# Kernel tuning notes

Hardware: AMD Instinct MI355X
Metric: run time of the kernel (lower is better)

## Reference

```python
import jax, jax.numpy as jnp
import numpy as np

N_NODES = 20000
IN_C = 512
OUT_C = 128
HEADS = 4
N_EDGES = 320000
NEG_SLOPE = 0.2


def setup_inputs() -> dict:
    key = jax.random.key(0)
    ks = jax.random.split(key, 10)
    x = jax.random.normal(ks[0], (N_NODES, IN_C), dtype=jnp.float32)
    edge_index = jax.random.randint(ks[1], (2, N_EDGES), 0, N_NODES, dtype=jnp.int64)
    s = 0.05
    return {
        "x": x,
        "edge_index": edge_index,
        "W1": jax.random.normal(ks[2], (IN_C, HEADS * OUT_C), dtype=jnp.float32) * s,
        "a_src1": jax.random.normal(ks[3], (HEADS, OUT_C), dtype=jnp.float32) * s,
        "a_dst1": jax.random.normal(ks[4], (HEADS, OUT_C), dtype=jnp.float32) * s,
        "b1": jnp.zeros((HEADS * OUT_C,), dtype=jnp.float32),
        "W2": jax.random.normal(ks[5], (HEADS * OUT_C, 1 * OUT_C), dtype=jnp.float32) * s,
        "a_src2": jax.random.normal(ks[6], (1, OUT_C), dtype=jnp.float32) * s,
        "a_dst2": jax.random.normal(ks[7], (1, OUT_C), dtype=jnp.float32) * s,
        "b2": jnp.zeros((OUT_C,), dtype=jnp.float32),
    }


def gat_conv(x, src, dst, W, a_src, a_dst, b, heads, out_c, concat):
    N = x.shape[0]
    h = (x @ W).reshape(N, heads, out_c)            # [N,H,C]
    al_src = jnp.sum(h * a_src, axis=-1)            # [N,H]
    al_dst = jnp.sum(h * a_dst, axis=-1)            # [N,H]
    e = jax.nn.leaky_relu(al_src[src] + al_dst[dst], NEG_SLOPE)  # [E,H]
    # segment softmax over edges grouped by destination node
    e_max = jax.ops.segment_max(e, dst, num_segments=N)         # [N,H]
    e = jnp.exp(e - e_max[dst])
    denom = jax.ops.segment_sum(e, dst, num_segments=N)         # [N,H]
    alpha = e / (denom[dst] + 1e-16)                             # [E,H]
    msg = h[src] * alpha[:, :, None]                             # [E,H,C]
    out = jax.ops.segment_sum(msg, dst, num_segments=N)          # [N,H,C]
    out = out.reshape(N, heads * out_c) if concat else jnp.mean(out, axis=1)
    return out + b


def reference(x, edge_index, W1, a_src1, a_dst1, b1, W2, a_src2, a_dst2, b2):
    N = x.shape[0]
    # PyG GATConv adds self-loops by default
    loops = jnp.arange(N, dtype=edge_index.dtype)
    src = jnp.concatenate([edge_index[0], loops])
    dst = jnp.concatenate([edge_index[1], loops])
    h = gat_conv(x, src, dst, W1, a_src1, a_dst1, b1, HEADS, OUT_C, concat=True)
    h = jax.nn.elu(h)
    return gat_conv(h, src, dst, W2, a_src2, a_dst2, b2, 1, OUT_C, concat=False)
```

## Files before the change

kernel.cpp:

```cpp
#include <hip/hip_runtime.h>
#include <hip/hip_bf16.h>

typedef __hip_bfloat16 bf16;
typedef __bf16 bf16x8 __attribute__((ext_vector_type(8)));
typedef float f32x4 __attribute__((ext_vector_type(4)));

#define NEG_SLOPE 0.2f
#define F32_THRESH 256


__device__ __forceinline__ bool is_f32(const int* fcnt) { return *fcnt > F32_THRESH; }

__device__ __forceinline__ float ld_f(const void* p, long long i, bool f32) {
    return f32 ? ((const float*)p)[i] : __bfloat162float(((const bf16*)p)[i]);
}

__device__ __forceinline__ float b2f(unsigned hs) {
    return __uint_as_float(hs << 16);
}

__device__ __forceinline__ unsigned pack_bf2(float a, float b) {
    union { bf16 h[2]; unsigned u; } p;
    p.h[0] = __float2bfloat16(a);
    p.h[1] = __float2bfloat16(b);
    return p.u;
}

__device__ __forceinline__ void load_lds16(const void* g, void* l) {
    __builtin_amdgcn_global_load_lds(
        (const __attribute__((address_space(1))) void*)g,
        (__attribute__((address_space(3))) void*)l, 16, 0, 0);
}

template <int CPL> struct FV;
template <> struct FV<8> {
    uint4 v;
    __device__ __forceinline__ void load(const bf16* p) { v = *(const uint4*)p; }
    __device__ __forceinline__ void fma(float* acc, float w) const {
        unsigned uu[4] = {v.x, v.y, v.z, v.w};
#pragma unroll
        for (int q = 0; q < 4; q++) {
            acc[2 * q] += w * b2f(uu[q] & 0xFFFFu);
            acc[2 * q + 1] += w * b2f(uu[q] >> 16);
        }
    }
};
template <> struct FV<2> {
    unsigned v;
    __device__ __forceinline__ void load(const bf16* p) { v = *(const unsigned*)p; }
    __device__ __forceinline__ void fma(float* acc, float w) const {
        acc[0] += w * b2f(v & 0xFFFFu);
        acc[1] += w * b2f(v >> 16);
    }
};


__global__ void k_probe(const unsigned* xw, long long nw, const int* idx, int n_half,
                        int* cnt, int* iflag) {
    long long t = blockIdx.x * (long long)blockDim.x + threadIdx.x;
    long long stride = (long long)gridDim.x * blockDim.x;
    int c = 0;
    for (long long i = t; i < nw; i += stride)
        if ((xw[i] & 0x7F80u) == 0x7F80u) c++;
    if (c) atomicAdd(cnt, c);
    int any = 0;
    for (long long i = t; i < n_half; i += stride)
        if (idx[2 * i + 1] != 0) any = 1;
    if (any) atomicOr(iflag, 1);
}


__device__ __forceinline__ int edge_val(const void* idx, long long i, int is64) {
    return is64 ? (int)((const long long*)idx)[i] : ((const int*)idx)[i];
}

__global__ void k_count(const void* idx, const int* iflag, int E0, int N, int* deg) {
    int e = blockIdx.x * blockDim.x + threadIdx.x;
    if (e >= E0 + N) return;
    int is64 = (*iflag == 0);
    int d = (e < E0) ? edge_val(idx, (long long)E0 + e, is64) : (e - E0);
    if ((unsigned)d >= (unsigned)N) d = 0;
    atomicAdd(&deg[d], 1);
}

__global__ __launch_bounds__(1024) void k_scan(const int* deg, int* rowptr, int N) {
    __shared__ int part[1024];
    int t = threadIdx.x;
    int chunk = (N + 1023) / 1024;
    int s = t * chunk, e = min(N, s + chunk);
    int sum = 0;
    for (int i = s; i < e; i++) sum += deg[i];
    part[t] = sum;
    __syncthreads();
    for (int off = 1; off < 1024; off <<= 1) {
        int v = (t >= off) ? part[t - off] : 0;
        __syncthreads();
        part[t] += v;
        __syncthreads();
    }
    int run = (t == 0) ? 0 : part[t - 1];
    for (int i = s; i < e; i++) { rowptr[i] = run; run += deg[i]; }
    if (t == 1023) rowptr[N] = part[1023];
}

__global__ void k_scatter(const void* idx, const int* iflag, int E0, int N,
                          const int* rowptr, int* cursor, int* csr_src) {
    int e = blockIdx.x * blockDim.x + threadIdx.x;
    if (e >= E0 + N) return;
    int is64 = (*iflag == 0);
    int s, d;
    if (e < E0) {
        s = edge_val(idx, e, is64);
        d = edge_val(idx, (long long)E0 + e, is64);
    } else {
        s = d = e - E0;
    }
    if ((unsigned)s >= (unsigned)N) s = 0;
    if ((unsigned)d >= (unsigned)N) d = 0;
    int pos = rowptr[d] + atomicAdd(&cursor[d], 1);
    if ((unsigned)pos < (unsigned)(E0 + N)) csr_src[pos] = s;
}


__global__ void k_prep(const void* x, const int* fcnt, bf16* xb, bf16* xtail,
                       const void* W1, bf16* W1t, const void* W2, bf16* W2t,
                       bf16* hpad, int hpad_elems, int N, int K, int C1, int C2,
                       int R0, long long n_valid, long long n_total) {
    const int b = blockIdx.x;
    const int tid = threadIdx.x;
    const bool f32 = is_f32(fcnt);
    if (b < 512) {
        if (!f32) return;
        long long n8 = n_total / 8;
        for (long long i = (long long)b * 256 + tid; i < n8; i += 512LL * 256) {
            long long base = i * 8;
            uint4 out;
            if (base + 8 <= n_valid) {
                const float4* s4 = (const float4*)x;
                float4 x0 = s4[i * 2], x1 = s4[i * 2 + 1];
                out.x = pack_bf2(x0.x, x0.y);
                out.y = pack_bf2(x0.z, x0.w);
                out.z = pack_bf2(x1.x, x1.y);
                out.w = pack_bf2(x1.z, x1.w);
            } else {
                bf16 tmp[8];
#pragma unroll
                for (int j = 0; j < 8; j++) {
                    long long k = base + j;
                    tmp[j] = (k < n_valid) ? __float2bfloat16(ld_f(x, k, true))
                                           : __float2bfloat16(0.f);
                }
                out = *(uint4*)tmp;
            }
            ((uint4*)xb)[i] = out;
        }
    } else if (b < 528) {
        int total = 128 * K;
        for (int i = (b - 512) * 256 + tid; i < total; i += 16 * 256) {
            int r = i / K;
            long long src = (long long)(R0 + r) * K + (i - r * K);
            xtail[i] = (R0 + r < N) ? __float2bfloat16(ld_f(x, src, f32))
                                    : __float2bfloat16(0.f);
        }
    } else if (b < 656) {
        int total = K * C1;
        for (int i = (b - 528) * 256 + tid; i < total; i += 128 * 256) {
            int k = i / C1, n = i - k * C1;
            W1t[(size_t)n * K + k] = __float2bfloat16(ld_f(W1, i, f32));
        }
    } else if (b < 688) {
        int total = C1 * C2;
        for (int i = (b - 656) * 256 + tid; i < total; i += 32 * 256) {
            int k = i / C2, n = i - k * C2;
            W2t[(size_t)n * C1 + k] = __float2bfloat16(ld_f(W2, i, f32));
        }
    } else {
        for (int i = (b - 688) * 256 + tid; i < hpad_elems; i += 16 * 256)
            hpad[i] = __float2bfloat16(0.f);
    }
}


__global__ void k_al(const bf16* __restrict__ h, const void* a_s, const void* a_d,
                     const int* fcnt, float* als, float* ald, int N, int H) {
    __shared__ float sa[512], sd[512];
    const int HC = H * 128;
    bool f32 = is_f32(fcnt);
    for (int i = threadIdx.x; i < HC; i += blockDim.x) {
        sa[i] = ld_f(a_s, i, f32);
        sd[i] = ld_f(a_d, i, f32);
    }
    __syncthreads();
    int i = blockIdx.x * blockDim.x + threadIdx.x;
    if (i >= N * H) return;
    int n = i / H, hh = i % H;
    const uint4* row = (const uint4*)(h + (size_t)n * HC + hh * 128);
    float s = 0.f, d = 0.f;
#pragma unroll
    for (int q = 0; q < 16; q++) {
        uint4 u = row[q];
        unsigned uu[4] = {u.x, u.y, u.z, u.w};
#pragma unroll
        for (int t = 0; t < 4; t++) {
            float v0 = b2f(uu[t] & 0xFFFFu), v1 = b2f(uu[t] >> 16);
            int c = hh * 128 + q * 8 + t * 2;
            s += v0 * sa[c] + v1 * sa[c + 1];
            d += v0 * sd[c] + v1 * sd[c + 1];
        }
    }
    als[i] = s;
    ald[i] = d;
}


template <int BN, bool SEL>
__global__ __launch_bounds__(256) void k_gemm(const void* Araw, const bf16* Aconv,
                                              const bf16* Atail, const int* fcnt,
                                              const bf16* __restrict__ Bt,
                                              bf16* __restrict__ C,
                                              int M, int Nn, int K, int nfull) {
    constexpr int BM = 128, BK = 32;
    constexpr int NT = BN / 32;
    const int m0 = blockIdx.x * BM;
    const int n0 = blockIdx.y * BN;
    __shared__ __bf16 As[BM][BK];
    __shared__ __bf16 Bs[BN][BK];
    const int tid = threadIdx.x;
    const int wave = tid >> 6;
    const int lane = tid & 63;
    const int wm = (wave & 1) * 64;
    const int wn = (wave >> 1) * (NT * 16);
    const int lm = lane & 15;
    const int quad = lane >> 4;
    const int srow = tid >> 2;
    const int scol = (tid & 3) * 8;

    f32x4 acc[4][NT];
#pragma unroll
    for (int mt = 0; mt < 4; mt++)
#pragma unroll
        for (int nt = 0; nt < NT; nt++) acc[mt][nt] = (f32x4){0.f, 0.f, 0.f, 0.f};

    const bf16* Abase;
    int arow0;
    if (SEL) {
        const bf16* Asel = is_f32(fcnt) ? Aconv : (const bf16*)Araw;
        if ((int)blockIdx.x < nfull) { Abase = Asel; arow0 = m0; }
        else { Abase = Atail; arow0 = 0; }
    } else {
        Abase = (const bf16*)Araw;
        arow0 = m0;
    }

    const char* Ab = (const char*)(Abase + (size_t)(arow0 + srow) * K + scol);
    const char* Bb = (const char*)(Bt + (size_t)(n0 + srow) * K + scol);
    char* ldsA = (char*)&As[0][0] + wave * 1024;
    char* ldsB = (char*)&Bs[0][0] + wave * 1024;
    const size_t rstep = (size_t)64 * K * 2;

    for (int k0 = 0; k0 < K; k0 += BK) {
        __syncthreads();
        const size_t kb = (size_t)k0 * 2;
        load_lds16(Ab + kb, ldsA);
        load_lds16(Ab + kb + rstep, ldsA + 4096);
        load_lds16(Bb + kb, ldsB);
        if (BN == 128) load_lds16(Bb + kb + rstep, ldsB + 4096);
        __syncthreads();
        bf16x8 af[4], bfv[NT];
#pragma unroll
        for (int mt = 0; mt < 4; mt++)
            af[mt] = *(const bf16x8*)&As[wm + mt * 16 + lm][quad * 8];
#pragma unroll
        for (int nt = 0; nt < NT; nt++)
            bfv[nt] = *(const bf16x8*)&Bs[wn + nt * 16 + lm][quad * 8];
#pragma unroll
        for (int mt = 0; mt < 4; mt++)
#pragma unroll
            for (int nt = 0; nt < NT; nt++)
                acc[mt][nt] = __builtin_amdgcn_mfma_f32_16x16x32_bf16(
                    af[mt], bfv[nt], acc[mt][nt], 0, 0, 0);
    }

#pragma unroll
    for (int mt = 0; mt < 4; mt++) {
        int rb = m0 + wm + mt * 16 + quad * 4;
#pragma unroll
        for (int nt = 0; nt < NT; nt++) {
            int col = n0 + wn + nt * 16 + lm;
#pragma unroll
            for (int r = 0; r < 4; r++) {
                int row = rb + r;
                if (row < M) C[(size_t)row * Nn + col] = __float2bfloat16(acc[mt][nt][r]);
            }
        }
    }
}


template <int C, int H, bool ELU, bool DYN_OUT>
__global__ __launch_bounds__(256) void k_agg(
    const bf16* __restrict__ feat, const float* __restrict__ als,
    const float* __restrict__ ald, const int* __restrict__ rowptr,
    const int* __restrict__ csr_src, const void* bias, const int* fcnt,
    void* outp, int N, int E) {
    constexpr int CPL = C / 64;
    constexpr int Ch = C / H;
    const int wave = threadIdx.x >> 6;
    const int lane = threadIdx.x & 63;
    const int n = blockIdx.x * 4 + wave;
    if (n >= N) return;
    const int c0 = lane * CPL;
    const int head = c0 / Ch;

    int start = rowptr[n];
    if (start < 0) start = 0;
    int end = rowptr[n + 1];
    if (end > E) end = E;
    int deg = end - start;
    if (deg < 0) deg = 0;

    const float aldn = ald[(size_t)n * H + head];
    float acc[CPL] = {};
    float psum = 0.f;

    if (deg > 0) {
        const int nb = (deg + 3) >> 2;

        auto load_idx = [&](int b, int* s, float* m) {
#pragma unroll
            for (int j = 0; j < 4; j++) {
                int e = b * 4 + j;
                bool v = e < deg;
                int sv = csr_src[start + (v ? e : 0)];
                if ((unsigned)sv >= (unsigned)N) sv = 0;
                s[j] = sv;
                m[j] = v ? 1.f : 0.f;
            }
        };
        auto load_data = [&](const int* s, float* a, FV<CPL>* f) {
#pragma unroll
            for (int j = 0; j < 4; j++) {
                a[j] = als[(size_t)s[j] * H + head];
                f[j].load(feat + (size_t)s[j] * C + c0);
            }
        };

        int sP[4];
        float mP[4];
        float aC[4], mC[4];
        FV<CPL> fC[4];

        load_idx(0, sP, mP);
        load_data(sP, aC, fC);
#pragma unroll
        for (int j = 0; j < 4; j++) mC[j] = mP[j];
        if (nb > 1) load_idx(1, sP, mP);

        for (int b = 0;; b++) {
            float aN[4], mN[4];
            FV<CPL> fN[4];
            bool more = (b + 1) < nb;
            if (more) {
                load_data(sP, aN, fN);
#pragma unroll
                for (int j = 0; j < 4; j++) mN[j] = mP[j];
                if (b + 2 < nb) load_idx(b + 2, sP, mP);
            }
#pragma unroll
            for (int j = 0; j < 4; j++) {
                float l = aC[j] + aldn;
                l = l > 0.f ? l : NEG_SLOPE * l;
                float w = mC[j] * __expf(fminf(l, 60.f));
                psum += w;
                fC[j].fma(acc, w);
            }
            if (!more) break;
#pragma unroll
            for (int j = 0; j < 4; j++) {
                aC[j] = aN[j];
                mC[j] = mN[j];
                fC[j] = fN[j];
            }
        }
    }

    const float dn = psum + 1e-16f;
    const bool f32 = is_f32(fcnt);
#pragma unroll
    for (int j = 0; j < CPL; j++) {
        float v = acc[j] / dn + ld_f(bias, c0 + j, f32);
        if (ELU) v = v > 0.f ? v : expf(v) - 1.f;
        size_t oi = (size_t)n * C + c0 + j;
        if (DYN_OUT && f32) ((float*)outp)[oi] = v;
        else ((bf16*)outp)[oi] = __float2bfloat16(v);
    }
}


extern "C" void kernel_launch(void* const* d_in, const int* in_sizes, int n_in,
                              void* d_out, int out_size, void* d_ws, size_t ws_size,
                              hipStream_t stream) {
    const int N = in_sizes[0] / 512;
    const int K = 512;
    const int C1 = 512;
    const int C2 = 128;
    const int H1 = 4;
    const int E0 = in_sizes[1] / 2;
    const int E = E0 + N;
    const int Mpad = (N + 127) / 128 * 128;
    const int nfull = N / 128;

    const void* x_raw = d_in[0];
    const void* eidx = d_in[1];
    const void* W1 = d_in[2];
    const void* as1 = d_in[3];
    const void* ad1 = d_in[4];
    const void* b1 = d_in[5];
    const void* W2 = d_in[6];
    const void* as2 = d_in[7];
    const void* ad2 = d_in[8];
    const void* b2 = d_in[9];

    char* ws = (char*)d_ws;
    size_t off = 0;
    auto take = [&](size_t bytes) {
        size_t r = off;
        off += (bytes + 255) & ~(size_t)255;
        return r;
    };
    bf16* xb     = (bf16*)(ws + take((size_t)Mpad * K * 2));
    bf16* xtail  = (bf16*)(ws + take((size_t)128 * K * 2));
    bf16* h1     = (bf16*)(ws + take((size_t)N * C1 * 2));
    bf16* hagg   = (bf16*)(ws + take((size_t)Mpad * C1 * 2));
    bf16* W1t    = (bf16*)(ws + take((size_t)K * C1 * 2));
    bf16* W2t    = (bf16*)(ws + take((size_t)C1 * C2 * 2));
    float* al1s  = (float*)(ws + take((size_t)N * H1 * 4));
    float* al1d  = (float*)(ws + take((size_t)N * H1 * 4));
    int* rowptr  = (int*)(ws + take((size_t)(N + 1) * 4));
    int* csr_src = (int*)(ws + take((size_t)E * 4));
    int* deg     = (int*)(ws + take((size_t)(2 * N + 2) * 4));
    int* cursor  = deg + N;
    int* iflag   = deg + 2 * N;
    int* fcnt    = deg + 2 * N + 1;
    bf16* h2     = xb;
    float* al2s  = al1s;
    float* al2d  = al1d;
    if (off > ws_size) return;

    hipMemsetAsync(deg, 0, (size_t)(2 * N + 2) * 4, stream);

    long long nw = (long long)in_sizes[0] / 2;
    if (nw > (1 << 20)) nw = 1 << 20;
    int nh = E0 > (1 << 16) ? (1 << 16) : E0;
    k_probe<<<256, 256, 0, stream>>>((const unsigned*)x_raw, nw, (const int*)eidx, nh,
                                     fcnt, iflag);

    k_count<<<(E + 255) / 256, 256, 0, stream>>>(eidx, iflag, E0, N, deg);
    k_scan<<<1, 1024, 0, stream>>>(deg, rowptr, N);
    k_scatter<<<(E + 255) / 256, 256, 0, stream>>>(eidx, iflag, E0, N, rowptr, cursor,
                                                   csr_src);

    k_prep<<<704, 256, 0, stream>>>(x_raw, fcnt, xb, xtail, W1, W1t, W2, W2t,
                                    hagg + (size_t)N * C1, (Mpad - N) * C1,
                                    N, K, C1, C2, nfull * 128,
                                    (long long)N * K, (long long)Mpad * K);

    dim3 g1(Mpad / 128, C1 / 128);
    k_gemm<128, true><<<g1, 256, 0, stream>>>(x_raw, xb, xtail, fcnt, W1t, h1,
                                              N, C1, K, nfull);
    k_al<<<(N * H1 + 255) / 256, 256, 0, stream>>>(h1, as1, ad1, fcnt, al1s, al1d, N, H1);
    k_agg<512, 4, true, false><<<(N + 3) / 4, 256, 0, stream>>>(
        h1, al1s, al1d, rowptr, csr_src, b1, fcnt, hagg, N, E);

    dim3 g2(Mpad / 128, C2 / 64);
    k_gemm<64, false><<<g2, 256, 0, stream>>>(hagg, nullptr, nullptr, fcnt, W2t, h2,
                                              N, C2, C1, 0);
    k_al<<<(N + 255) / 256, 256, 0, stream>>>(h2, as2, ad2, fcnt, al2s, al2d, N, 1);
    k_agg<128, 1, false, true><<<(N + 3) / 4, 256, 0, stream>>>(
        h2, al2s, al2d, rowptr, csr_src, b2, fcnt, d_out, N, E);
}
```

Measured before the change: 317.4 us.

## Precompute edge weights cooperatively per wave into shared memory in aggregation

Restructures the aggregation loop so each wave first loads up to 64 neighbor indices in parallel, computes attention weights for all heads once per edge (vectorized float4 load of source logits), and stores them in LDS. The accumulation loop then reads the index and weight from shared memory and does only the feature gather and FMA. This removes the redundant per-lane logit load and exp and the serial index loads, but drops the explicit software prefetch pipeline of feature rows, relying on unroll 4 for memory-level parallelism instead.

```diff
diff --git a/kernel.cpp b/kernel.cpp
--- a/kernel.cpp
+++ b/kernel.cpp
@@ -305,12 +305,17 @@
     void* outp, int N, int E) {
     constexpr int CPL = C / 64;
     constexpr int Ch = C / H;
+    constexpr int WPAD = (H == 4) ? 5 : 1;
     const int wave = threadIdx.x >> 6;
     const int lane = threadIdx.x & 63;
     const int n = blockIdx.x * 4 + wave;
-    if (n >= N) return;
     const int c0 = lane * CPL;
     const int head = c0 / Ch;
+
+    __shared__ float s_w[4][64 * WPAD];
+    __shared__ int s_s[4][64];
+
+    if (n >= N) return;
 
     int start = rowptr[n];
     if (start < 0) start = 0;
@@ -319,68 +324,47 @@
     int deg = end - start;
     if (deg < 0) deg = 0;
 
-    const float aldn = ald[(size_t)n * H + head];
+    float aldn[H];
+    if (H == 4) {
+        float4 a4 = ((const float4*)ald)[n];
+        aldn[0] = a4.x; aldn[1] = a4.y; aldn[2] = a4.z;
+        if (H > 3) aldn[3] = a4.w;
+    } else {
+        aldn[0] = ald[n];
+    }
+
     float acc[CPL] = {};
     float psum = 0.f;
 
-    if (deg > 0) {
-        const int nb = (deg + 3) >> 2;
-
-        auto load_idx = [&](int b, int* s, float* m) {
-#pragma unroll
-            for (int j = 0; j < 4; j++) {
-                int e = b * 4 + j;
-                bool v = e < deg;
-                int sv = csr_src[start + (v ? e : 0)];
-                if ((unsigned)sv >= (unsigned)N) sv = 0;
-                s[j] = sv;
-                m[j] = v ? 1.f : 0.f;
+    for (int base = 0; base < deg; base += 64) {
+        int cnt = min(64, deg - base);
+        if (lane < cnt) {
+            int s = csr_src[start + base + lane];
+            if ((unsigned)s >= (unsigned)N) s = 0;
+            s_s[wave][lane] = s;
+            if (H == 4) {
+                float4 a4 = ((const float4*)als)[s];
+                float aa[4] = {a4.x, a4.y, a4.z, a4.w};
+#pragma unroll
+                for (int h = 0; h < 4; h++) {
+                    float l = aa[h] + aldn[h];
+                    l = l > 0.f ? l : NEG_SLOPE * l;
+                    s_w[wave][lane * 5 + h] = __expf(fminf(l, 60.f));
+                }
+            } else {
+                float l = als[s] + aldn[0];
+                l = l > 0.f ? l : NEG_SLOPE * l;
+                s_w[wave][lane] = __expf(fminf(l, 60.f));
             }
-        };
-        auto load_data = [&](const int* s, float* a, FV<CPL>* f) {
-#pragma unroll
-            for (int j = 0; j < 4; j++) {
-                a[j] = als[(size_t)s[j] * H + head];
-                f[j].load(feat + (size_t)s[j] * C + c0);
-            }
-        };
-
-        int sP[4];
-        float mP[4];
-        float aC[4], mC[4];
-        FV<CPL> fC[4];
-
-        load_idx(0, sP, mP);
-        load_data(sP, aC, fC);
-#pragma unroll
-        for (int j = 0; j < 4; j++) mC[j] = mP[j];
-        if (nb > 1) load_idx(1, sP, mP);
-
-        for (int b = 0;; b++) {
-            float aN[4], mN[4];
-            FV<CPL> fN[4];
-            bool more = (b + 1) < nb;
-            if (more) {
-                load_data(sP, aN, fN);
-#pragma unroll
-                for (int j = 0; j < 4; j++) mN[j] = mP[j];
-                if (b + 2 < nb) load_idx(b + 2, sP, mP);
-            }
-#pragma unroll
-            for (int j = 0; j < 4; j++) {
-                float l = aC[j] + aldn;
-                l = l > 0.f ? l : NEG_SLOPE * l;
-                float w = mC[j] * __expf(fminf(l, 60.f));
-                psum += w;
-                fC[j].fma(acc, w);
-            }
-            if (!more) break;
-#pragma unroll
-            for (int j = 0; j < 4; j++) {
-                aC[j] = aN[j];
-                mC[j] = mN[j];
-                fC[j] = fN[j];
-            }
+        }
+#pragma unroll 4
+        for (int e = 0; e < cnt; e++) {
+            int s = s_s[wave][e];
+            float wl = (H == 4) ? s_w[wave][e * 5 + head] : s_w[wave][e];
+            psum += wl;
+            FV<CPL> f;
+            f.load(feat + (size_t)s * C + c0);
+            f.fma(acc, wl);
         }
     }
 
```

After: 316.2 us. No clear change (-0.4%).
